# Kernel tuning notes

Measured on AMD Instinct MI355X. Metric: run time of the kernel, lower is better.

## Reference

```python
import jax, jax.numpy as jnp
import numpy as np

N, F, H, E, G, C = 100000, 128, 128, 640000, 512, 6
EPS = 1e-5


def setup_inputs() -> dict:
    key = jax.random.key(0)
    ks = jax.random.split(key, 20)
    def w(k, shape, fan_in):
        return jax.random.normal(k, shape, jnp.float32) * (1.0 / np.sqrt(fan_in))
    return {
        "x": jax.random.normal(ks[0], (N, F), jnp.float32),
        "edge_index": jax.random.randint(ks[1], (2, E), 0, N),
        "batch": jnp.sort(jax.random.randint(ks[2], (N,), 0, G)),
        "num_graphs": G,
        # SAGEConv1: lin_l (aggregated, with bias) + lin_r (root, no bias)
        "W1l": w(ks[3], (F, H), F), "b1l": jnp.zeros((H,), jnp.float32), "W1r": w(ks[4], (F, H), F),
        # SAGEConv2
        "W2l": w(ks[5], (H, H), H), "b2l": jnp.zeros((H,), jnp.float32), "W2r": w(ks[6], (H, H), H),
        # cluster heads
        "Wc1": w(ks[7], (H, H), H), "bc1": jnp.zeros((H,), jnp.float32),
        "Wc2": w(ks[8], (H, 2), H), "bc2": jnp.zeros((2,), jnp.float32),
        # classifier
        "Wl1": w(ks[9], (H, H), H), "bl1": jnp.zeros((H,), jnp.float32),
        "Wl2": w(ks[10], (H, C), H), "bl2": jnp.zeros((C,), jnp.float32),
    }


def _sage(x, src, dst, Wl, bl, Wr):
    # PyG SAGEConv: mean-aggregate messages x[src] at dst, then lin_l(agg) + lin_r(x)
    n = x.shape[0]
    s = jax.ops.segment_sum(x[src], dst, num_segments=n)
    cnt = jax.ops.segment_sum(jnp.ones((src.shape[0],), x.dtype), dst, num_segments=n)
    agg = s / jnp.maximum(cnt, 1.0)[:, None]
    return agg @ Wl + bl + x @ Wr


def reference(x, edge_index, batch, num_graphs,
              W1l, b1l, W1r, W2l, b2l, W2r,
              Wc1, bc1, Wc2, bc2, Wl1, bl1, Wl2, bl2):
    src, dst = edge_index[0], edge_index[1]
    h = jax.nn.relu(_sage(x, src, dst, W1l, b1l, W1r))
    h = jax.nn.relu(_sage(h, src, dst, W2l, b2l, W2r))
    # 2-way soft cluster assignment per node
    a = jax.nn.softmax(jnp.tanh(h @ Wc1 + bc1) @ Wc2 + bc2, axis=1)  # [N,2]
    g = num_graphs
    # group_features[g] = a_g^T h_g  -> per-node outer product, segment-summed by graph
    gf = jax.ops.segment_sum(a[:, :, None] * h[:, None, :], batch, num_segments=g)  # [G,2,H]
    pos = gf[:, 0, :]  # positive-cluster embedding per graph
    # new_adj[g] = a_g^T A_g a_g ; only within-graph edges appear in the per-graph adj block
    same = (batch[src] == batch[dst]).astype(h.dtype)
    contrib = same[:, None, None] * (a[src][:, :, None] * a[dst][:, None, :])  # [E,2,2]
    new_adj = jax.ops.segment_sum(contrib, batch[src], num_segments=g)  # [G,2,2]
    # F.normalize(p=1, dim=1, eps=1e-5): row-wise L1 with clamped denominator
    l1 = jnp.sum(jnp.abs(new_adj), axis=2, keepdims=True)
    norm_adj = new_adj / jnp.maximum(l1, EPS)
    diag = jnp.diagonal(norm_adj, axis1=1, axis2=2)  # [G,2]
    penalty = jnp.mean(jnp.mean((diag - 1.0) ** 2, axis=1))  # mse vs ones(2), averaged over graphs
    # NOTE: original (faithfully reproduced) takes the mean over ALL nodes, same for every graph
    graph_emb = jnp.broadcast_to(jnp.mean(h, axis=0, keepdims=True), (g, h.shape[1]))
    z = jax.nn.relu(pos @ Wl1 + bl1)  # dropout off (eval mode)
    logits = z @ Wl2 + bl2
    return (jax.nn.log_softmax(logits, axis=-1), pos, graph_emb, penalty)
```

## Files before the change

kernel.cpp:

```cpp
#include <hip/hip_runtime.h>

#define NN 100000
#define NE 640000
#define HD 128
#define NG 512
#define NC 6
#define EPSV 1e-5f
#define OCT 12500

typedef __bf16 bf16_t;
typedef bf16_t bf16x8 __attribute__((ext_vector_type(8)));
typedef float f32x4 __attribute__((ext_vector_type(4)));

__device__ __forceinline__ float b2f(unsigned int u16) {
    return __builtin_bit_cast(float, u16 << 16);
}
__device__ __forceinline__ unsigned short f2b(float f) {
    unsigned int u = __builtin_bit_cast(unsigned int, f);
    unsigned int r = (u + 0x7fffu + ((u >> 16) & 1u)) >> 16;
    return (unsigned short)r;
}

__device__ __forceinline__ int frag_src_h(int i, int h) {
    int g2 = i >> 6, ln = i & 63;
    int row = (h * 4 + (g2 >> 2)) * 16 + (ln & 15);
    return row * 16 + (g2 & 3) * 4 + (ln >> 4);
}

__device__ __forceinline__ int frag_src(int i) {
    int g2 = i >> 6, ln = i & 63;
    int row = (g2 >> 2) * 16 + (ln & 15);
    return row * 16 + (g2 & 3) * 4 + (ln >> 4);
}

__global__ __launch_bounds__(256) void k_zero(uint4* __restrict__ p, int n16) {
    int i = blockIdx.x * 256 + threadIdx.x;
    if (i < n16) p[i] = (uint4){0u, 0u, 0u, 0u};
}

__global__ __launch_bounds__(256) void k_prep(
    const float* __restrict__ x, unsigned short* __restrict__ xb,
    const float* __restrict__ Wa, const float* __restrict__ Wb,
    const float* __restrict__ Wc, const float* __restrict__ Wd,
    const float* __restrict__ We, unsigned short* __restrict__ Wt,
    const int* __restrict__ dst, int* __restrict__ cnt)
{
    int bid = blockIdx.x;
    if (bid < 960) {
        int oct = bid & 7;
        int widx = bid >> 3;
        int lo = oct * OCT, hi = lo + OCT;
        for (int e = widx * 256 + threadIdx.x; e < NE; e += 120 * 256) {
            int d = dst[e];
            if (d >= lo && d < hi) atomicAdd(&cnt[d], 1);
        }
    } else if (bid < 7210) {
        int i = (bid - 960) * 256 + threadIdx.x;
        float4 v0 = reinterpret_cast<const float4*>(x)[i * 2];
        float4 v1 = reinterpret_cast<const float4*>(x)[i * 2 + 1];
        unsigned short u[8] = {f2b(v0.x), f2b(v0.y), f2b(v0.z), f2b(v0.w),
                               f2b(v1.x), f2b(v1.y), f2b(v1.z), f2b(v1.w)};
        reinterpret_cast<uint4*>(xb)[i] = *reinterpret_cast<uint4*>(u);
    } else {
        int i = (bid - 7210) * 256 + threadIdx.x;
        int w = i >> 14, r = i & 16383;
        int k = r >> 7, n = r & 127;
        const float* W = (w == 0) ? Wa : (w == 1) ? Wb : (w == 2) ? Wc : (w == 3) ? Wd : We;
        Wt[w * 16384 + n * HD + k] = f2b(W[k * HD + n]);
    }
}

__global__ void k_scan1(const int* __restrict__ cnt, int* __restrict__ excl,
                        int* __restrict__ bsum, int n) {
    __shared__ int sh[256];
    int i = blockIdx.x * 256 + threadIdx.x;
    int v = (i < n) ? cnt[i] : 0;
    sh[threadIdx.x] = v;
    __syncthreads();
    for (int off = 1; off < 256; off <<= 1) {
        int t = (threadIdx.x >= off) ? sh[threadIdx.x - off] : 0;
        __syncthreads();
        sh[threadIdx.x] += t;
        __syncthreads();
    }
    if (i < n) excl[i] = sh[threadIdx.x] - v;
    if (threadIdx.x == 255) bsum[blockIdx.x] = sh[255];
}

__global__ void k_scan2(int* bsum, int nb) {
    __shared__ int sh[512];
    int t = threadIdx.x;
    sh[t] = (t < nb) ? bsum[t] : 0;
    __syncthreads();
    for (int off = 1; off < 512; off <<= 1) {
        int v = (t >= off) ? sh[t - off] : 0;
        __syncthreads();
        sh[t] += v;
        __syncthreads();
    }
    if (t < nb) bsum[t] = sh[t];
}

__global__ void k_scan3(const int* __restrict__ excl, const int* __restrict__ bsum,
                        int* __restrict__ row_off, int n) {
    int i = blockIdx.x * 256 + threadIdx.x;
    if (i < n) row_off[i] = excl[i] + (blockIdx.x ? bsum[blockIdx.x - 1] : 0);
    if (i == 0) row_off[n] = NE;
}

__global__ __launch_bounds__(256) void k_fill(const int* __restrict__ src,
                                              const int* __restrict__ dst,
                                              const int* __restrict__ row_off,
                                              int* __restrict__ cnt,
                                              int* __restrict__ csr) {
    int q = blockIdx.x;
    int oct = q & 7;
    int widx = q >> 3;
    int lo = oct * OCT, hi = lo + OCT;
    for (int e = widx * 256 + threadIdx.x; e < NE; e += 120 * 256) {
        int d = dst[e];
        if (d >= lo && d < hi) {
            int p = atomicSub(&cnt[d], 1);
            csr[row_off[d] + p - 1] = src[e];
        }
    }
}

__global__ __launch_bounds__(512) void k_sage(
    const unsigned short* __restrict__ X,
    const int* __restrict__ row_off, const int* __restrict__ csr,
    const unsigned short* __restrict__ Wlt, const unsigned short* __restrict__ Wrt,
    const float* __restrict__ bias, unsigned short* __restrict__ out, int M)
{
    __shared__ uint4 wlds[2048];
    const int wid = threadIdx.x >> 6;
    const int lane = threadIdx.x & 63;
    const int lrow = lane & 15;
    const int lkg = lane >> 4;
    const int r0 = blockIdx.x * 128 + wid * 16;

    const uint4* gl = reinterpret_cast<const uint4*>(Wlt);
    const uint4* gr = reinterpret_cast<const uint4*>(Wrt);
    for (int i = threadIdx.x; i < 1024; i += 512) {
        wlds[i] = gl[frag_src_h(i, 0)];
        wlds[1024 + i] = gr[frag_src_h(i, 0)];
    }

    int row = r0 + lrow;
    row = row < M ? row : M - 1;
    int beg = row_off[row], end = row_off[row + 1];

    float accg[4][8];
#pragma unroll
    for (int ks = 0; ks < 4; ++ks)
#pragma unroll
        for (int j = 0; j < 8; ++j) accg[ks][j] = 0.f;

    const unsigned short* Xk = X + lkg * 8;
    for (int j = beg; j < end; j += 2) {
        int s0 = csr[j];
        const unsigned short* p0 = Xk + (size_t)s0 * HD;
        uint4 w0 = *reinterpret_cast<const uint4*>(p0);
        uint4 w1 = *reinterpret_cast<const uint4*>(p0 + 32);
        uint4 w2 = *reinterpret_cast<const uint4*>(p0 + 64);
        uint4 w3 = *reinterpret_cast<const uint4*>(p0 + 96);
        bool ok1 = (j + 1) < end;
        int s1 = csr[ok1 ? j + 1 : j];
        const unsigned short* p1 = Xk + (size_t)s1 * HD;
        uint4 y0, y1, y2, y3;
        if (ok1) {
            y0 = *reinterpret_cast<const uint4*>(p1);
            y1 = *reinterpret_cast<const uint4*>(p1 + 32);
            y2 = *reinterpret_cast<const uint4*>(p1 + 64);
            y3 = *reinterpret_cast<const uint4*>(p1 + 96);
        }
        accg[0][0] += b2f(w0.x & 0xffffu); accg[0][1] += b2f(w0.x >> 16);
        accg[0][2] += b2f(w0.y & 0xffffu); accg[0][3] += b2f(w0.y >> 16);
        accg[0][4] += b2f(w0.z & 0xffffu); accg[0][5] += b2f(w0.z >> 16);
        accg[0][6] += b2f(w0.w & 0xffffu); accg[0][7] += b2f(w0.w >> 16);
        accg[1][0] += b2f(w1.x & 0xffffu); accg[1][1] += b2f(w1.x >> 16);
        accg[1][2] += b2f(w1.y & 0xffffu); accg[1][3] += b2f(w1.y >> 16);
        accg[1][4] += b2f(w1.z & 0xffffu); accg[1][5] += b2f(w1.z >> 16);
        accg[1][6] += b2f(w1.w & 0xffffu); accg[1][7] += b2f(w1.w >> 16);
        accg[2][0] += b2f(w2.x & 0xffffu); accg[2][1] += b2f(w2.x >> 16);
        accg[2][2] += b2f(w2.y & 0xffffu); accg[2][3] += b2f(w2.y >> 16);
        accg[2][4] += b2f(w2.z & 0xffffu); accg[2][5] += b2f(w2.z >> 16);
        accg[2][6] += b2f(w2.w & 0xffffu); accg[2][7] += b2f(w2.w >> 16);
        accg[3][0] += b2f(w3.x & 0xffffu); accg[3][1] += b2f(w3.x >> 16);
        accg[3][2] += b2f(w3.y & 0xffffu); accg[3][3] += b2f(w3.y >> 16);
        accg[3][4] += b2f(w3.z & 0xffffu); accg[3][5] += b2f(w3.z >> 16);
        accg[3][6] += b2f(w3.w & 0xffffu); accg[3][7] += b2f(w3.w >> 16);
        if (ok1) {
            accg[0][0] += b2f(y0.x & 0xffffu); accg[0][1] += b2f(y0.x >> 16);
            accg[0][2] += b2f(y0.y & 0xffffu); accg[0][3] += b2f(y0.y >> 16);
            accg[0][4] += b2f(y0.z & 0xffffu); accg[0][5] += b2f(y0.z >> 16);
            accg[0][6] += b2f(y0.w & 0xffffu); accg[0][7] += b2f(y0.w >> 16);
            accg[1][0] += b2f(y1.x & 0xffffu); accg[1][1] += b2f(y1.x >> 16);
            accg[1][2] += b2f(y1.y & 0xffffu); accg[1][3] += b2f(y1.y >> 16);
            accg[1][4] += b2f(y1.z & 0xffffu); accg[1][5] += b2f(y1.z >> 16);
            accg[1][6] += b2f(y1.w & 0xffffu); accg[1][7] += b2f(y1.w >> 16);
            accg[2][0] += b2f(y2.x & 0xffffu); accg[2][1] += b2f(y2.x >> 16);
            accg[2][2] += b2f(y2.y & 0xffffu); accg[2][3] += b2f(y2.y >> 16);
            accg[2][4] += b2f(y2.z & 0xffffu); accg[2][5] += b2f(y2.z >> 16);
            accg[2][6] += b2f(y2.w & 0xffffu); accg[2][7] += b2f(y2.w >> 16);
            accg[3][0] += b2f(y3.x & 0xffffu); accg[3][1] += b2f(y3.x >> 16);
            accg[3][2] += b2f(y3.y & 0xffffu); accg[3][3] += b2f(y3.y >> 16);
            accg[3][4] += b2f(y3.z & 0xffffu); accg[3][5] += b2f(y3.z >> 16);
            accg[3][6] += b2f(y3.w & 0xffffu); accg[3][7] += b2f(y3.w >> 16);
        }
    }

    float inv = 1.f / fmaxf((float)(end - beg), 1.f);
    bf16x8 a1[4], a2f[4];
#pragma unroll
    for (int ks = 0; ks < 4; ++ks) {
        unsigned short u[8];
#pragma unroll
        for (int j = 0; j < 8; ++j) u[j] = f2b(accg[ks][j] * inv);
        a1[ks] = *reinterpret_cast<bf16x8*>(u);
    }
    const unsigned short* p2 = X + (size_t)row * HD + lkg * 8;
#pragma unroll
    for (int ks = 0; ks < 4; ++ks)
        a2f[ks] = *reinterpret_cast<const bf16x8*>(p2 + ks * 32);

    {
        f32x4 acc[4];
#pragma unroll
        for (int t = 0; t < 4; ++t) {
            float b = bias[t * 16 + lrow];
            acc[t] = (f32x4){b, b, b, b};
        }
        __syncthreads();
#pragma unroll
        for (int ks = 0; ks < 4; ++ks) {
#pragma unroll
            for (int t = 0; t < 4; ++t) {
                int fi = (t * 4 + ks) * 64 + lane;
                bf16x8 bl = __builtin_bit_cast(bf16x8, wlds[fi]);
                bf16x8 br = __builtin_bit_cast(bf16x8, wlds[1024 + fi]);
                acc[t] = __builtin_amdgcn_mfma_f32_16x16x32_bf16(a1[ks], bl, acc[t], 0, 0, 0);
                acc[t] = __builtin_amdgcn_mfma_f32_16x16x32_bf16(a2f[ks], br, acc[t], 0, 0, 0);
            }
        }
#pragma unroll
        for (int t = 0; t < 4; ++t)
#pragma unroll
            for (int r = 0; r < 4; ++r) {
                int orow = r0 + lkg * 4 + r;
                if (orow < M)
                    out[(size_t)orow * HD + t * 16 + lrow] = f2b(fmaxf(acc[t][r], 0.f));
            }
    }

    __syncthreads();
    for (int i = threadIdx.x; i < 1024; i += 512) {
        wlds[i] = gl[frag_src_h(i, 1)];
        wlds[1024 + i] = gr[frag_src_h(i, 1)];
    }
    {
        f32x4 acc[4];
#pragma unroll
        for (int t = 0; t < 4; ++t) {
            float b = bias[(4 + t) * 16 + lrow];
            acc[t] = (f32x4){b, b, b, b};
        }
        __syncthreads();
#pragma unroll
        for (int ks = 0; ks < 4; ++ks) {
#pragma unroll
            for (int t = 0; t < 4; ++t) {
                int fi = (t * 4 + ks) * 64 + lane;
                bf16x8 bl = __builtin_bit_cast(bf16x8, wlds[fi]);
                bf16x8 br = __builtin_bit_cast(bf16x8, wlds[1024 + fi]);
                acc[t] = __builtin_amdgcn_mfma_f32_16x16x32_bf16(a1[ks], bl, acc[t], 0, 0, 0);
                acc[t] = __builtin_amdgcn_mfma_f32_16x16x32_bf16(a2f[ks], br, acc[t], 0, 0, 0);
            }
        }
#pragma unroll
        for (int t = 0; t < 4; ++t)
#pragma unroll
            for (int r = 0; r < 4; ++r) {
                int orow = r0 + lkg * 4 + r;
                if (orow < M)
                    out[(size_t)orow * HD + (4 + t) * 16 + lrow] = f2b(fmaxf(acc[t][r], 0.f));
            }
    }
}

__global__ __launch_bounds__(256) void mfma_attn(
    const unsigned short* __restrict__ A1, const unsigned short* __restrict__ W1t,
    const float* __restrict__ bias, const float* __restrict__ Wc2,
    const float* __restrict__ bc2, float* __restrict__ a2, int M)
{
    __shared__ uint4 wlds[2048];
    const int wid = threadIdx.x >> 6;
    const int lane = threadIdx.x & 63;
    const int lrow = lane & 15;
    const int lkg = lane >> 4;
    const int r0 = blockIdx.x * 128 + wid * 32;

    const uint4* g4 = reinterpret_cast<const uint4*>(W1t);
    for (int i = threadIdx.x; i < 2048; i += 256)
        wlds[i] = g4[frag_src(i)];

    bf16x8 a[2][4];
#pragma unroll
    for (int g = 0; g < 2; ++g) {
        int row = r0 + g * 16 + lrow;
        row = row < M ? row : M - 1;
        const unsigned short* p = A1 + (size_t)row * HD + lkg * 8;
#pragma unroll
        for (int ks = 0; ks < 4; ++ks)
            a[g][ks] = *reinterpret_cast<const bf16x8*>(p + ks * 32);
    }

    f32x4 acc[2][8];
#pragma unroll
    for (int t = 0; t < 8; ++t) {
        float b = bias[t * 16 + lrow];
        acc[0][t] = (f32x4){b, b, b, b};
        acc[1][t] = (f32x4){b, b, b, b};
    }

    __syncthreads();

#pragma unroll
    for (int ks = 0; ks < 4; ++ks) {
#pragma unroll
        for (int t = 0; t < 8; ++t) {
            bf16x8 b = __builtin_bit_cast(bf16x8, wlds[(t * 4 + ks) * 64 + lane]);
            acc[0][t] = __builtin_amdgcn_mfma_f32_16x16x32_bf16(a[0][ks], b, acc[0][t], 0, 0, 0);
            acc[1][t] = __builtin_amdgcn_mfma_f32_16x16x32_bf16(a[1][ks], b, acc[1][t], 0, 0, 0);
        }
    }

    float p0[2][4] = {{0.f, 0.f, 0.f, 0.f}, {0.f, 0.f, 0.f, 0.f}};
    float p1[2][4] = {{0.f, 0.f, 0.f, 0.f}, {0.f, 0.f, 0.f, 0.f}};
#pragma unroll
    for (int t = 0; t < 8; ++t) {
        float2 wv = reinterpret_cast<const float2*>(Wc2)[t * 16 + lrow];
#pragma unroll
        for (int g = 0; g < 2; ++g)
#pragma unroll
            for (int r = 0; r < 4; ++r) {
                float tv = tanhf(acc[g][t][r]);
                p0[g][r] = fmaf(tv, wv.x, p0[g][r]);
                p1[g][r] = fmaf(tv, wv.y, p1[g][r]);
            }
    }
#pragma unroll
    for (int off = 1; off < 16; off <<= 1) {
#pragma unroll
        for (int g = 0; g < 2; ++g)
#pragma unroll
            for (int r = 0; r < 4; ++r) {
                p0[g][r] += __shfl_xor(p0[g][r], off, 64);
                p1[g][r] += __shfl_xor(p1[g][r], off, 64);
            }
    }
    if (lrow == 0) {
        float B0 = bc2[0], B1 = bc2[1];
#pragma unroll
        for (int g = 0; g < 2; ++g)
#pragma unroll
            for (int r = 0; r < 4; ++r) {
                int row = r0 + g * 16 + lkg * 4 + r;
                if (row < M) {
                    float u0 = p0[g][r] + B0, u1 = p1[g][r] + B1;
                    float m = fmaxf(u0, u1);
                    float e0 = expf(u0 - m), e1 = expf(u1 - m);
                    float inv = 1.f / (e0 + e1);
                    reinterpret_cast<float2*>(a2)[row] = (float2){e0 * inv, e1 * inv};
                }
            }
    }
}

__global__ __launch_bounds__(1024) void k_posadj(const unsigned short* __restrict__ h,
                                                 const float* __restrict__ a2,
                                                 const int* __restrict__ batch,
                                                 const int* __restrict__ src,
                                                 const int* __restrict__ dst,
                                                 float* __restrict__ pos_out,
                                                 float* __restrict__ csum,
                                                 float* __restrict__ adj) {
    __shared__ float4 sh[16][64];
    __shared__ float shadj[NG * 4];
    int bid = blockIdx.x;
    if (bid < NG) {
        int g = bid;
        int lo = 0, hi = NN;
        while (lo < hi) { int m = (lo + hi) >> 1; if (batch[m] < g) lo = m + 1; else hi = m; }
        int beg = lo;
        hi = NN;
        while (lo < hi) { int m = (lo + hi) >> 1; if (batch[m] < g + 1) lo = m + 1; else hi = m; }
        int end = lo;
        int grp = threadIdx.x >> 6;
        int lane = threadIdx.x & 63;
        float4 acc = {0.f, 0.f, 0.f, 0.f};
        for (int i = beg + grp * 2; i < end; i += 32) {
            int i1 = i + 1;
            bool ok1 = i1 < end;
            float a0 = a2[i * 2];
            unsigned int v0 = *reinterpret_cast<const unsigned int*>(h + (size_t)i * HD + lane * 2);
            float a1 = ok1 ? a2[i1 * 2] : 0.f;
            unsigned int v1 = ok1 ? *reinterpret_cast<const unsigned int*>(h + (size_t)i1 * HD + lane * 2) : 0u;
            float f0 = b2f(v0 & 0xffffu), f1 = b2f(v0 >> 16);
            float g0 = b2f(v1 & 0xffffu), g1 = b2f(v1 >> 16);
            acc.x = fmaf(a0, f0, fmaf(a1, g0, acc.x));
            acc.y = fmaf(a0, f1, fmaf(a1, g1, acc.y));
            acc.z += f0 + g0;
            acc.w += f1 + g1;
        }
        sh[grp][lane] = acc;
        __syncthreads();
        if (threadIdx.x < 64) {
            float4 s = sh[0][lane];
#pragma unroll
            for (int k = 1; k < 16; ++k) {
                float4 t = sh[k][lane];
                s.x += t.x; s.y += t.y; s.z += t.z; s.w += t.w;
            }
            reinterpret_cast<float2*>(pos_out)[g * 64 + lane] = (float2){s.x, s.y};
            atomicAdd(&csum[lane * 2], s.z);
            atomicAdd(&csum[lane * 2 + 1], s.w);
        }
    } else {
        for (int i = threadIdx.x; i < NG * 4; i += 1024) shadj[i] = 0.f;
        __syncthreads();
        for (int e = (bid - NG) * 1024 + threadIdx.x; e < NE; e += 120 * 1024) {
            int s = src[e], d = dst[e];
            int bs = batch[s], bd = batch[d];
            if (bs != bd) continue;
            float a0s = a2[2 * s], a1s = a2[2 * s + 1];
            float a0d = a2[2 * d], a1d = a2[2 * d + 1];
            float* A = shadj + bs * 4;
            atomicAdd(A + 0, a0s * a0d);
            atomicAdd(A + 1, a0s * a1d);
            atomicAdd(A + 2, a1s * a0d);
            atomicAdd(A + 3, a1s * a1d);
        }
        __syncthreads();
        for (int i = threadIdx.x; i < NG * 4; i += 1024) {
            float v = shadj[i];
            if (v != 0.f) atomicAdd(&adj[i], v);
        }
    }
}

__global__ __launch_bounds__(512) void k_tail(const float* __restrict__ csum,
                                              float* __restrict__ gemb_out,
                                              const float* __restrict__ adj,
                                              float* __restrict__ pen) {
    int bid = blockIdx.x;
    if (bid < 128) {
        int i = bid * 512 + threadIdx.x;
        gemb_out[i] = csum[i & 127] * (1.f / (float)NN);
    } else {
        __shared__ float sh[512];
        int g = threadIdx.x;
        float x0 = adj[g * 4], x1 = adj[g * 4 + 1], x2 = adj[g * 4 + 2], x3 = adj[g * 4 + 3];
        float l0 = fabsf(x0) + fabsf(x1);
        float l1 = fabsf(x2) + fabsf(x3);
        float d0 = x0 / fmaxf(l0, EPSV);
        float d1 = x3 / fmaxf(l1, EPSV);
        sh[g] = 0.5f * ((d0 - 1.f) * (d0 - 1.f) + (d1 - 1.f) * (d1 - 1.f));
        __syncthreads();
        for (int off = 256; off >= 1; off >>= 1) {
            if (g < off) sh[g] += sh[g + off];
            __syncthreads();
        }
        if (g == 0) pen[0] = sh[0] * (1.f / (float)NG);
    }
}

__global__ __launch_bounds__(256) void gemm_head(
    const float* __restrict__ A, const float* __restrict__ W,
    const float* __restrict__ bias, float* __restrict__ out, int M)
{
    const int tid = threadIdx.x;
    const int w = __builtin_amdgcn_readfirstlane(tid >> 6);
    const int lane = tid & 63;
    const int r0 = blockIdx.x * 32 + w * 8;
    if (r0 >= M) return;
    const int c0 = lane, c1 = lane + 64;
    float acc0[8], acc1[8];
    const float b0 = bias[c0], b1 = bias[c1];
#pragma unroll
    for (int r = 0; r < 8; ++r) { acc0[r] = b0; acc1[r] = b1; }
    const float* Ap = A + (size_t)r0 * HD;
    for (int k4 = 0; k4 < HD / 4; ++k4) {
        float4 a[8];
#pragma unroll
        for (int r = 0; r < 8; ++r)
            a[r] = *reinterpret_cast<const float4*>(Ap + r * HD + k4 * 4);
#pragma unroll
        for (int j = 0; j < 4; ++j) {
            const int k = k4 * 4 + j;
            const float w0 = W[k * HD + c0];
            const float w1 = W[k * HD + c1];
#pragma unroll
            for (int r = 0; r < 8; ++r) {
                const float av = (j == 0) ? a[r].x : (j == 1) ? a[r].y
                               : (j == 2) ? a[r].z : a[r].w;
                acc0[r] = fmaf(av, w0, acc0[r]);
                acc1[r] = fmaf(av, w1, acc1[r]);
            }
        }
    }
#pragma unroll
    for (int r = 0; r < 8; ++r) {
        out[(size_t)(r0 + r) * HD + c0] = fmaxf(acc0[r], 0.f);
        out[(size_t)(r0 + r) * HD + c1] = fmaxf(acc1[r], 0.f);
    }
}

__global__ void k_head(const float* __restrict__ z, const float* __restrict__ Wl2,
                       const float* __restrict__ bl2, float* __restrict__ out0) {
    int g = blockIdx.x * blockDim.x + threadIdx.x;
    if (g >= NG) return;
    float l[NC];
#pragma unroll
    for (int c = 0; c < NC; ++c) l[c] = bl2[c];
    for (int k = 0; k < HD; ++k) {
        float zv = z[(size_t)g * HD + k];
#pragma unroll
        for (int c = 0; c < NC; ++c) l[c] = fmaf(zv, Wl2[k * NC + c], l[c]);
    }
    float m = l[0];
#pragma unroll
    for (int c = 1; c < NC; ++c) m = fmaxf(m, l[c]);
    float sum = 0.f;
#pragma unroll
    for (int c = 0; c < NC; ++c) sum += expf(l[c] - m);
    float lse = m + logf(sum);
#pragma unroll
    for (int c = 0; c < NC; ++c) out0[g * NC + c] = l[c] - lse;
}

extern "C" void kernel_launch(void* const* d_in, const int* in_sizes, int n_in,
                              void* d_out, int out_size, void* d_ws, size_t ws_size,
                              hipStream_t stream) {
    const float* x   = (const float*)d_in[0];
    const int*   ei  = (const int*)d_in[1];
    const int*   src = ei;
    const int*   dst = ei + NE;
    const int*   batch = (const int*)d_in[2];
    const float* W1l = (const float*)d_in[4];
    const float* b1l = (const float*)d_in[5];
    const float* W1r = (const float*)d_in[6];
    const float* W2l = (const float*)d_in[7];
    const float* b2l = (const float*)d_in[8];
    const float* W2r = (const float*)d_in[9];
    const float* Wc1 = (const float*)d_in[10];
    const float* bc1 = (const float*)d_in[11];
    const float* Wc2 = (const float*)d_in[12];
    const float* bc2 = (const float*)d_in[13];
    const float* Wl1 = (const float*)d_in[14];
    const float* bl1 = (const float*)d_in[15];
    const float* Wl2 = (const float*)d_in[16];
    const float* bl2 = (const float*)d_in[17];

    char* ws = (char*)d_ws;
    const size_t BB = (size_t)NN * HD * 2;
    unsigned short* xb   = (unsigned short*)(ws);
    unsigned short* bufB = (unsigned short*)(ws + BB);
    size_t O = 2 * BB;
    int*   cnt     = (int*)(ws + O);
    float* adj     = (float*)(ws + O + 400000);
    float* csum    = (float*)(ws + O + 408192);
    int*   row_off = (int*)(ws + O + 408704);
    int*   excl    = (int*)(ws + O + 808768);
    int*   bsum    = (int*)(ws + O + 1208768);
    int*   csr     = (int*)(ws + O + 1212864);
    float* a2      = (float*)(ws + O + 3772864);
    float* zbuf    = (float*)(ws + O + 4572864);
    unsigned short* w1lt = (unsigned short*)(ws + O + 4835008);
    unsigned short* w1rt = w1lt + 16384;
    unsigned short* w2lt = w1rt + 16384;
    unsigned short* w2rt = w2lt + 16384;
    unsigned short* wc1t = w2rt + 16384;

    float* out0 = (float*)d_out;
    float* pos  = out0 + NG * NC;
    float* gemb = pos + NG * HD;
    float* pen  = gemb + NG * HD;

    k_zero<<<100, 256, 0, stream>>>((uint4*)(ws + O), 25544);
    k_prep<<<7530, 256, 0, stream>>>(x, xb, W1l, W1r, W2l, W2r, Wc1, w1lt, dst, cnt);
    k_scan1<<<391, 256, 0, stream>>>(cnt, excl, bsum, NN);
    k_scan2<<<1, 512, 0, stream>>>(bsum, 391);
    k_scan3<<<391, 256, 0, stream>>>(excl, bsum, row_off, NN);
    k_fill<<<960, 256, 0, stream>>>(src, dst, row_off, cnt, csr);

    const int SAGE_GRID = (NN + 127) / 128;
    k_sage<<<SAGE_GRID, 512, 0, stream>>>(xb, row_off, csr, w1lt, w1rt, b1l, bufB, NN);
    k_sage<<<SAGE_GRID, 512, 0, stream>>>(bufB, row_off, csr, w2lt, w2rt, b2l, xb, NN);
    mfma_attn<<<(NN + 127) / 128, 256, 0, stream>>>(xb, wc1t, bc1, Wc2, bc2, a2, NN);
    k_posadj<<<NG + 120, 1024, 0, stream>>>(xb, a2, batch, src, dst, pos, csum, adj);
    k_tail<<<129, 512, 0, stream>>>(csum, gemb, adj, pen);
    gemm_head<<<NG / 32, 256, 0, stream>>>(pos, Wl1, bl1, zbuf, NG);
    k_head<<<2, 256, 0, stream>>>(zbuf, Wl2, bl2, out0);
}
```

Measured before the change: 276.2 us.

## Sort SAGE rows by in-degree to balance per-wave gather loop lengths

Builds a degree histogram and a counting-sort permutation of nodes (descending degree), then the SAGE kernels process rows in permuted order and scatter outputs to the original row positions. This is meant to reduce divergence within each 16-row wave, where the loop runs to the largest degree in the group, and to balance work across blocks. It adds three small kernels with global atomics, an extra indirection per row, and scattered output writes that lose the contiguity of rows within a tile.

```diff
diff --git a/kernel.cpp b/kernel.cpp
--- a/kernel.cpp
+++ b/kernel.cpp
@@ -26,7 +26,6 @@
     int row = (h * 4 + (g2 >> 2)) * 16 + (ln & 15);
     return row * 16 + (g2 & 3) * 4 + (ln >> 4);
 }
-
 __device__ __forceinline__ int frag_src(int i) {
     int g2 = i >> 6, ln = i & 63;
     int row = (g2 >> 2) * 16 + (ln & 15);
@@ -70,6 +69,29 @@
     }
 }
 
+__global__ void k_hist(const int* __restrict__ cnt, int* __restrict__ hist, int n) {
+    int i = blockIdx.x * 256 + threadIdx.x;
+    if (i < n) {
+        int bin = cnt[i] < 63 ? cnt[i] : 63;
+        atomicAdd(&hist[bin], 1);
+    }
+}
+__global__ void k_hscan(const int* __restrict__ hist, int* __restrict__ hoff) {
+    int b = threadIdx.x;
+    int s = 0;
+    for (int j = b + 1; j < 64; ++j) s += hist[j];
+    hoff[b] = s;
+}
+__global__ void k_scatter(const int* __restrict__ cnt, int* __restrict__ hoff,
+                          int* __restrict__ perm, int n) {
+    int i = blockIdx.x * 256 + threadIdx.x;
+    if (i < n) {
+        int bin = cnt[i] < 63 ? cnt[i] : 63;
+        int p = atomicAdd(&hoff[bin], 1);
+        perm[p] = i;
+    }
+}
+
 __global__ void k_scan1(const int* __restrict__ cnt, int* __restrict__ excl,
                         int* __restrict__ bsum, int n) {
     __shared__ int sh[256];
@@ -129,6 +151,7 @@
 __global__ __launch_bounds__(512) void k_sage(
     const unsigned short* __restrict__ X,
     const int* __restrict__ row_off, const int* __restrict__ csr,
+    const int* __restrict__ perm,
     const unsigned short* __restrict__ Wlt, const unsigned short* __restrict__ Wrt,
     const float* __restrict__ bias, unsigned short* __restrict__ out, int M)
 {
@@ -146,9 +169,19 @@
         wlds[1024 + i] = gr[frag_src_h(i, 0)];
     }
 
-    int row = r0 + lrow;
-    row = row < M ? row : M - 1;
+    int idx = r0 + lrow;
+    idx = idx < M ? idx : M - 1;
+    int row = perm[idx];
     int beg = row_off[row], end = row_off[row + 1];
+
+    int pr[4];
+    bool pv[4];
+#pragma unroll
+    for (int r = 0; r < 4; ++r) {
+        int oi = r0 + lkg * 4 + r;
+        pv[r] = oi < M;
+        pr[r] = perm[pv[r] ? oi : M - 1];
+    }
 
     float accg[4][8];
 #pragma unroll
@@ -246,11 +279,9 @@
 #pragma unroll
         for (int t = 0; t < 4; ++t)
 #pragma unroll
-            for (int r = 0; r < 4; ++r) {
-                int orow = r0 + lkg * 4 + r;
-                if (orow < M)
-                    out[(size_t)orow * HD + t * 16 + lrow] = f2b(fmaxf(acc[t][r], 0.f));
-            }
+            for (int r = 0; r < 4; ++r)
+                if (pv[r])
+                    out[(size_t)pr[r] * HD + t * 16 + lrow] = f2b(fmaxf(acc[t][r], 0.f));
     }
 
     __syncthreads();
@@ -280,11 +311,9 @@
 #pragma unroll
         for (int t = 0; t < 4; ++t)
 #pragma unroll
-            for (int r = 0; r < 4; ++r) {
-                int orow = r0 + lkg * 4 + r;
-                if (orow < M)
-                    out[(size_t)orow * HD + (4 + t) * 16 + lrow] = f2b(fmaxf(acc[t][r], 0.f));
-            }
+            for (int r = 0; r < 4; ++r)
+                if (pv[r])
+                    out[(size_t)pr[r] * HD + (4 + t) * 16 + lrow] = f2b(fmaxf(acc[t][r], 0.f));
     }
 }
 
@@ -570,13 +599,16 @@
     int*   cnt     = (int*)(ws + O);
     float* adj     = (float*)(ws + O + 400000);
     float* csum    = (float*)(ws + O + 408192);
-    int*   row_off = (int*)(ws + O + 408704);
-    int*   excl    = (int*)(ws + O + 808768);
-    int*   bsum    = (int*)(ws + O + 1208768);
-    int*   csr     = (int*)(ws + O + 1212864);
-    float* a2      = (float*)(ws + O + 3772864);
-    float* zbuf    = (float*)(ws + O + 4572864);
-    unsigned short* w1lt = (unsigned short*)(ws + O + 4835008);
+    int*   hist    = (int*)(ws + O + 408704);
+    int*   hoff    = (int*)(ws + O + 408960);
+    int*   row_off = (int*)(ws + O + 409216);
+    int*   excl    = (int*)(ws + O + 809280);
+    int*   bsum    = (int*)(ws + O + 1209280);
+    int*   csr     = (int*)(ws + O + 1213376);
+    float* a2      = (float*)(ws + O + 3773376);
+    float* zbuf    = (float*)(ws + O + 4573376);
+    int*   perm    = (int*)(ws + O + 4835520);
+    unsigned short* w1lt = (unsigned short*)(ws + O + 5235520);
     unsigned short* w1rt = w1lt + 16384;
     unsigned short* w2lt = w1rt + 16384;
     unsigned short* w2rt = w2lt + 16384;
@@ -587,16 +619,19 @@
     float* gemb = pos + NG * HD;
     float* pen  = gemb + NG * HD;
 
-    k_zero<<<100, 256, 0, stream>>>((uint4*)(ws + O), 25544);
+    k_zero<<<100, 256, 0, stream>>>((uint4*)(ws + O), 25576);
     k_prep<<<7530, 256, 0, stream>>>(x, xb, W1l, W1r, W2l, W2r, Wc1, w1lt, dst, cnt);
+    k_hist<<<391, 256, 0, stream>>>(cnt, hist, NN);
+    k_hscan<<<1, 64, 0, stream>>>(hist, hoff);
+    k_scatter<<<391, 256, 0, stream>>>(cnt, hoff, perm, NN);
     k_scan1<<<391, 256, 0, stream>>>(cnt, excl, bsum, NN);
     k_scan2<<<1, 512, 0, stream>>>(bsum, 391);
     k_scan3<<<391, 256, 0, stream>>>(excl, bsum, row_off, NN);
     k_fill<<<960, 256, 0, stream>>>(src, dst, row_off, cnt, csr);
 
     const int SAGE_GRID = (NN + 127) / 128;
-    k_sage<<<SAGE_GRID, 512, 0, stream>>>(xb, row_off, csr, w1lt, w1rt, b1l, bufB, NN);
-    k_sage<<<SAGE_GRID, 512, 0, stream>>>(bufB, row_off, csr, w2lt, w2rt, b2l, xb, NN);
+    k_sage<<<SAGE_GRID, 512, 0, stream>>>(xb, row_off, csr, perm, w1lt, w1rt, b1l, bufB, NN);
+    k_sage<<<SAGE_GRID, 512, 0, stream>>>(bufB, row_off, csr, perm, w2lt, w2rt, b2l, xb, NN);
     mfma_attn<<<(NN + 127) / 128, 256, 0, stream>>>(xb, wc1t, bc1, Wc2, bc2, a2, NN);
     k_posadj<<<NG + 120, 1024, 0, stream>>>(xb, a2, batch, src, dst, pos, csum, adj);
     k_tail<<<129, 512, 0, stream>>>(csum, gemb, adj, pen);
```

After: 987.8 us. +257.6%, slower.
